# Optimization experiments

Hardware: AMD Instinct MI355X
Metric: run time of the kernel (lower is better)

Reference implementation:

```python
import jax, jax.numpy as jnp
import numpy as np

NUM_HEADS = 32
HEAD_DIM = 128
HIDDEN = NUM_HEADS * HEAD_DIM  # 4096
PAGE_SIZE = 16
NUM_PHYS_PAGES = 512
CACHE_POS = 4096
BATCH = 32
SEQ = 1


def setup_inputs() -> dict:
    key = jax.random.key(0)
    ks = jax.random.split(key, 6)
    scale = 0.02
    x = jax.random.normal(ks[0], (BATCH, SEQ, HIDDEN), dtype=jnp.float32)
    w_qkv = jax.random.normal(ks[1], (HIDDEN, 3 * HIDDEN), dtype=jnp.float32) * scale
    b_qkv = jnp.zeros((3 * HIDDEN,), dtype=jnp.float32)
    w_proj = jax.random.normal(ks[2], (HIDDEN, HIDDEN), dtype=jnp.float32) * scale
    b_proj = jnp.zeros((HIDDEN,), dtype=jnp.float32)
    k_pages = jax.random.normal(ks[3], (NUM_PHYS_PAGES, PAGE_SIZE, NUM_HEADS, HEAD_DIM), dtype=jnp.float32)
    v_pages = jax.random.normal(ks[4], (NUM_PHYS_PAGES, PAGE_SIZE, NUM_HEADS, HEAD_DIM), dtype=jnp.float32)
    # logical page -> physical page mapping (page table for one request)
    page_table = jax.random.randint(ks[5], (CACHE_POS // PAGE_SIZE,), 0, NUM_PHYS_PAGES, dtype=jnp.int64)
    return {
        "x": x, "w_qkv": w_qkv, "b_qkv": b_qkv, "w_proj": w_proj, "b_proj": b_proj,
        "k_pages": k_pages, "v_pages": v_pages, "page_table": page_table,
        "cache_pos": CACHE_POS,
    }


def reference(x, w_qkv, b_qkv, w_proj, b_proj, k_pages, v_pages, page_table, cache_pos):
    B, S, H = x.shape
    # fused QKV projection
    qkv = x @ w_qkv + b_qkv                      # [B,S,3H]
    q, k, v = jnp.split(qkv, 3, axis=-1)
    q = q.reshape(B, S, NUM_HEADS, HEAD_DIM).transpose(0, 2, 1, 3)  # [B,Hh,S,D]
    k = k.reshape(B, S, NUM_HEADS, HEAD_DIM).transpose(0, 2, 1, 3)
    v = v.reshape(B, S, NUM_HEADS, HEAD_DIM).transpose(0, 2, 1, 3)

    # Paged KV-cache gather: position -> (physical page, local offset)
    pos = jnp.arange(cache_pos)                  # cache_pos is a static Python int
    phys = page_table[pos // PAGE_SIZE]          # [T]
    off = pos % PAGE_SIZE                        # [T]
    cached_k = k_pages[phys, off]                # [T, Hh, D]
    cached_v = v_pages[phys, off]                # [T, Hh, D]
    # [1,Hh,T,D], shared across batch (as in the torch expand)
    cached_k = jnp.transpose(cached_k, (1, 0, 2))[None]
    cached_v = jnp.transpose(cached_v, (1, 0, 2))[None]
    cached_k = jnp.broadcast_to(cached_k, (B,) + cached_k.shape[1:])
    cached_v = jnp.broadcast_to(cached_v, (B,) + cached_v.shape[1:])

    k_full = jnp.concatenate([cached_k, k], axis=2)  # [B,Hh,T+S,D]
    v_full = jnp.concatenate([cached_v, v], axis=2)

    scores = jnp.einsum('bhsd,bhtd->bhst', q, k_full) / (HEAD_DIM ** 0.5)
    attn = jax.nn.softmax(scores, axis=-1)
    out = jnp.einsum('bhst,bhtd->bhsd', attn, v_full)  # [B,Hh,S,D]
    out = out.transpose(0, 2, 1, 3).reshape(B, S, H)
    return out @ w_proj + b_proj
```

## Files before the change

### kernel.cpp

```cpp
#include <hip/hip_runtime.h>

typedef __attribute__((ext_vector_type(4))) float f32x4;
typedef __attribute__((ext_vector_type(8))) short short8;
typedef unsigned short u16;
typedef unsigned int u32;

#define HEADS 32
#define D 128
#define TCACHE 4096
#define HID 4096
#define QKVN 12288
#define TSPLIT 32
#define KPS (TCACHE / TSPLIT)
#define QKV_KSPLIT 4
#define PROJ_KSPLIT 8
#define SCALE 0.08838834764831845f
#define ARENA_W 10880

static __device__ __forceinline__ float bf2f(u16 u) {
  u32 v = ((u32)u) << 16;
  return __builtin_bit_cast(float, v);
}
static __device__ __forceinline__ u16 f2bf(float f) {
  u32 u = __builtin_bit_cast(u32, f);
  u += 0x7FFFu + ((u >> 16) & 1u);
  return (u16)(u >> 16);
}

template <bool BF>
static __device__ __forceinline__ short8 load8(const void* p, long idx) {
  if constexpr (BF) {
    return *(const short8*)((const u16*)p + idx);
  } else {
    const float* f = (const float*)p + idx;
    f32x4 a = *(const f32x4*)f;
    f32x4 b = *(const f32x4*)(f + 4);
    short8 r;
    r[0] = (short)f2bf(a[0]); r[1] = (short)f2bf(a[1]);
    r[2] = (short)f2bf(a[2]); r[3] = (short)f2bf(a[3]);
    r[4] = (short)f2bf(b[0]); r[5] = (short)f2bf(b[1]);
    r[6] = (short)f2bf(b[2]); r[7] = (short)f2bf(b[3]);
    return r;
  }
}
template <bool BF>
static __device__ __forceinline__ short ld1(const void* p, long idx) {
  if constexpr (BF) return (short)((const u16*)p)[idx];
  else return (short)f2bf(((const float*)p)[idx]);
}

__global__ void prep(const u32* __restrict__ x, const u32* __restrict__ raw,
                     int* __restrict__ flag, int* __restrict__ ptn) {
  if (blockIdx.x == 0) {
    __shared__ int cnt;
    if (threadIdx.x == 0) cnt = 0;
    __syncthreads();
    u32 v = x[threadIdx.x * 256];
    u32 e = (v >> 7) & 0xFF;
    if (e >= 110 && e <= 140) atomicAdd(&cnt, 1);
    __syncthreads();
    if (threadIdx.x == 0) *flag = (cnt >= 192) ? 1 : 0;
  } else {
    __shared__ int is64;
    if (threadIdx.x == 0) is64 = 1;
    __syncthreads();
    if (threadIdx.x < 128) {
      u32 odd = raw[2 * threadIdx.x + 1];
      if (odd != 0) atomicAnd(&is64, 0);
    }
    __syncthreads();
    if (is64) ptn[threadIdx.x] = (int)raw[2 * threadIdx.x];
    else ptn[threadIdx.x] = (int)raw[threadIdx.x];
  }
}

template <bool ABF, bool BBF>
static __device__ __forceinline__ void gemm_body(const void* __restrict__ A,
                                                 const void* __restrict__ B,
                                                 float* __restrict__ C, int K, int N) {
  int wave = threadIdx.x >> 6, lane = threadIdx.x & 63;
  int l16 = lane & 15, lg = lane >> 4;
  int n0 = blockIdx.x * 64 + wave * 16;
  int kper = K / gridDim.y;
  int k0 = blockIdx.y * kper;
  f32x4 acc0 = {0.f, 0.f, 0.f, 0.f}, acc1 = {0.f, 0.f, 0.f, 0.f};
  long arow0 = (long)l16 * K, arow1 = (long)(l16 + 16) * K;
#pragma unroll 4
  for (int kk = k0; kk < k0 + kper; kk += 32) {
    long kbase = kk + lg * 8;
    short8 a0 = load8<ABF>(A, arow0 + kbase);
    short8 a1 = load8<ABF>(A, arow1 + kbase);
    short8 bfr;
#pragma unroll
    for (int i = 0; i < 8; i++) bfr[i] = ld1<BBF>(B, (kbase + i) * (long)N + n0 + l16);
    acc0 = __builtin_amdgcn_mfma_f32_16x16x32_bf16(a0, bfr, acc0, 0, 0, 0);
    acc1 = __builtin_amdgcn_mfma_f32_16x16x32_bf16(a1, bfr, acc1, 0, 0, 0);
  }
  float* Co = C + (long)blockIdx.y * 32 * N;
#pragma unroll
  for (int i = 0; i < 4; i++) {
    int b = lg * 4 + i;
    Co[(long)b * N + n0 + l16] = acc0[i];
    Co[(long)(b + 16) * N + n0 + l16] = acc1[i];
  }
}

#define GPITCH 36
static __device__ __forceinline__ void gemm32_body(const float* __restrict__ A,
                                                   const float* __restrict__ B,
                                                   float* __restrict__ C, int K, int N,
                                                   u16* __restrict__ BtL,
                                                   u16* __restrict__ AtL) {
  int t = threadIdx.x;
  int wave = t >> 6, lane = t & 63, l16 = lane & 15, lg = lane >> 4;
  int kper = K / gridDim.y;
  int k0 = blockIdx.y * kper;
  int steps = kper >> 5;
  long n0 = (long)blockIdx.x * 64;
  int bk = (t >> 4) * 2;
  int bc = (t & 15) * 4;
  int am = t >> 3;
  int ak = (t & 7) * 4;
  f32x4 acc0 = {0.f, 0.f, 0.f, 0.f}, acc1 = {0.f, 0.f, 0.f, 0.f};
  f32x4 rb0, rb1, ra;

  auto LOADG = [&](int kk) {
    const float* Bp = B + (long)(k0 + kk + bk) * N + n0 + bc;
    rb0 = *(const f32x4*)Bp;
    rb1 = *(const f32x4*)(Bp + N);
    ra = *(const f32x4*)(A + (long)am * K + k0 + kk + ak);
  };
  auto STORE = [&](int buf) {
    u16* Bt = BtL + buf * (64 * GPITCH);
#pragma unroll
    for (int c = 0; c < 4; c++) {
      u32 w = (u32)f2bf(rb0[c]) | ((u32)f2bf(rb1[c]) << 16);
      *(u32*)(Bt + (bc + c) * GPITCH + bk) = w;
    }
    u16* At = AtL + buf * (32 * GPITCH);
    *(u32*)(At + am * GPITCH + ak) = (u32)f2bf(ra[0]) | ((u32)f2bf(ra[1]) << 16);
    *(u32*)(At + am * GPITCH + ak + 2) = (u32)f2bf(ra[2]) | ((u32)f2bf(ra[3]) << 16);
  };
  auto FRAGMFMA = [&](int buf) {
    union { short8 s8; u32 w[4]; } bf, af0, af1;
    const u32* bp = (const u32*)(BtL + buf * (64 * GPITCH) + ((wave * 16 + l16) * GPITCH + lg * 8));
    bf.w[0] = bp[0]; bf.w[1] = bp[1]; bf.w[2] = bp[2]; bf.w[3] = bp[3];
    const u32* a0p = (const u32*)(AtL + buf * (32 * GPITCH) + (l16 * GPITCH + lg * 8));
    af0.w[0] = a0p[0]; af0.w[1] = a0p[1]; af0.w[2] = a0p[2]; af0.w[3] = a0p[3];
    const u32* a1p = (const u32*)(AtL + buf * (32 * GPITCH) + ((l16 + 16) * GPITCH + lg * 8));
    af1.w[0] = a1p[0]; af1.w[1] = a1p[1]; af1.w[2] = a1p[2]; af1.w[3] = a1p[3];
    acc0 = __builtin_amdgcn_mfma_f32_16x16x32_bf16(af0.s8, bf.s8, acc0, 0, 0, 0);
    acc1 = __builtin_amdgcn_mfma_f32_16x16x32_bf16(af1.s8, bf.s8, acc1, 0, 0, 0);
  };

  LOADG(0);
  STORE(0);
  __syncthreads();
  for (int s = 0; s < steps; s++) {
    int cur = s & 1;
    bool more = (s + 1 < steps);
    if (more) LOADG((s + 1) * 32);
    FRAGMFMA(cur);
    if (more) STORE(cur ^ 1);
    __syncthreads();
  }
  float* Co = C + (long)blockIdx.y * 32 * N;
  long cw = n0 + wave * 16 + l16;
#pragma unroll
  for (int i = 0; i < 4; i++) {
    int b = lg * 4 + i;
    Co[(long)b * N + cw] = acc0[i];
    Co[(long)(b + 16) * N + cw] = acc1[i];
  }
}

__global__ __launch_bounds__(256) void qkv_gemm(const void* A, const void* B, float* C,
                                                const int* flag) {
  __shared__ u16 BtL[2 * 64 * GPITCH];
  __shared__ u16 AtL[2 * 32 * GPITCH];
  if (*flag) gemm_body<true, true>(A, B, C, HID, QKVN);
  else gemm32_body((const float*)A, (const float*)B, C, HID, QKVN, BtL, AtL);
}
__global__ __launch_bounds__(256) void proj_gemm(const void* Abf, const void* Af32,
                                                 const void* B, float* C, const int* flag) {
  __shared__ u16 BtL[2 * 64 * GPITCH];
  __shared__ u16 AtL[2 * 32 * GPITCH];
  if (*flag) gemm_body<true, true>(Abf, B, C, HID, HID);
  else gemm32_body((const float*)Af32, (const float*)B, C, HID, HID, BtL, AtL);
}

__global__ void qkv_fin(const float* __restrict__ C, const void* __restrict__ bias,
                        u16* __restrict__ out, const int* __restrict__ flag) {
  int idx = blockIdx.x * 256 + threadIdx.x;
  if (idx >= 32 * QKVN) return;
  int n = idx % QKVN;
  float s = 0.f;
#pragma unroll
  for (int sp = 0; sp < QKV_KSPLIT; sp++) s += C[(long)sp * 32 * QKVN + idx];
  float bv;
  if (*flag) bv = bf2f(((const u16*)bias)[n]);
  else bv = ((const float*)bias)[n];
  out[idx] = f2bf(s + bv);
}

__global__ void proj_fin(const float* __restrict__ C, const void* __restrict__ bias,
                         void* __restrict__ out, const int* __restrict__ flag) {
  int idx = blockIdx.x * 256 + threadIdx.x;
  if (idx >= 32 * HID) return;
  int n = idx % HID;
  float s = 0.f;
#pragma unroll
  for (int sp = 0; sp < PROJ_KSPLIT; sp++) s += C[(long)sp * 32 * HID + idx];
  if (*flag) {
    s += bf2f(((const u16*)bias)[n]);
    ((u16*)out)[idx] = f2bf(s);
  } else {
    s += ((const float*)bias)[n];
    ((float*)out)[idx] = s;
  }
}

template <bool BF>
static __device__ __forceinline__ void attn_body(const u16* __restrict__ qkv,
                                                 const void* __restrict__ kp,
                                                 const void* __restrict__ vp,
                                                 const int* __restrict__ pt,
                                                 float* __restrict__ Op,
                                                 float* __restrict__ mp,
                                                 float* __restrict__ lp,
                                                 char* __restrict__ arena,
                                                 float (*mL)[32], float (*lL)[32]) {
  int split = blockIdx.x, h = blockIdx.y;
  int wave = threadIdx.x >> 6, lane = threadIdx.x & 63;
  int l16 = lane & 15, lg = lane >> 4;
  u16* VLw = (u16*)(arena + wave * ARENA_W);
  u16* pldsw = (u16*)(arena + wave * ARENA_W + 8320);

  short8 qf[2][4];
#pragma unroll
  for (int mt = 0; mt < 2; mt++)
#pragma unroll
    for (int ks = 0; ks < 4; ks++)
      qf[mt][ks] = *(const short8*)(qkv + (long)(l16 + 16 * mt) * QKVN + h * D + ks * 32 + lg * 8);

  f32x4 acc[2][8];
#pragma unroll
  for (int mt = 0; mt < 2; mt++)
#pragma unroll
    for (int nt = 0; nt < 8; nt++) acc[mt][nt] = f32x4{0.f, 0.f, 0.f, 0.f};
  float mrun[2][4], lrun[2][4];

  int tbase = split * KPS + wave * 32;
  int tb16 = tbase >> 4;
  int pg0 = pt[tb16], pg1 = pt[tb16 + 1];

#pragma unroll
  for (int p = 0; p < 2; p++) {
    int kc = (lane >> 2) + p * 16;
    int dq = (lane & 3) * 32;
    int pg = (kc & 16) ? pg1 : pg0;
    long vr = ((long)(pg * 16 + (kc & 15)) * HEADS + h) * D;
    u32 w[16];
    if constexpr (BF) {
      const u32* src = (const u32*)vp + ((vr + dq) >> 1);
#pragma unroll
      for (int j = 0; j < 16; j++) w[j] = src[j];
    } else {
      const float* src = (const float*)vp + vr + dq;
#pragma unroll
      for (int j = 0; j < 8; j++) {
        f32x4 tv = *(const f32x4*)(src + j * 4);
        w[2 * j] = (u32)f2bf(tv[0]) | ((u32)f2bf(tv[1]) << 16);
        w[2 * j + 1] = (u32)f2bf(tv[2]) | ((u32)f2bf(tv[3]) << 16);
      }
    }
    u32* dst = (u32*)(VLw + kc * 130 + dq);
#pragma unroll
    for (int j = 0; j < 16; j++) dst[j] = w[j];
  }

  f32x4 sacc[2][2];
#pragma unroll
  for (int kt = 0; kt < 2; kt++)
#pragma unroll
    for (int mt = 0; mt < 2; mt++) sacc[kt][mt] = f32x4{0.f, 0.f, 0.f, 0.f};
#pragma unroll
  for (int kt = 0; kt < 2; kt++) {
    long krow = ((long)((kt ? pg1 : pg0) * 16 + l16) * HEADS + h) * D;
#pragma unroll
    for (int ks = 0; ks < 4; ks++) {
      short8 kf = load8<BF>(kp, krow + ks * 32 + lg * 8);
      sacc[kt][0] = __builtin_amdgcn_mfma_f32_16x16x32_bf16(qf[0][ks], kf, sacc[kt][0], 0, 0, 0);
      sacc[kt][1] = __builtin_amdgcn_mfma_f32_16x16x32_bf16(qf[1][ks], kf, sacc[kt][1], 0, 0, 0);
    }
  }

  float p[2][2][4];
#pragma unroll
  for (int mt = 0; mt < 2; mt++) {
#pragma unroll
    for (int i = 0; i < 4; i++) {
      float s0 = sacc[0][mt][i] * SCALE, s1 = sacc[1][mt][i] * SCALE;
      float mx = fmaxf(s0, s1);
      mx = fmaxf(mx, __shfl_xor(mx, 1));
      mx = fmaxf(mx, __shfl_xor(mx, 2));
      mx = fmaxf(mx, __shfl_xor(mx, 4));
      mx = fmaxf(mx, __shfl_xor(mx, 8));
      float p0 = __expf(s0 - mx), p1 = __expf(s1 - mx);
      float ps = p0 + p1;
      ps += __shfl_xor(ps, 1);
      ps += __shfl_xor(ps, 2);
      ps += __shfl_xor(ps, 4);
      ps += __shfl_xor(ps, 8);
      mrun[mt][i] = mx;
      lrun[mt][i] = ps;
      p[0][mt][i] = p0;
      p[1][mt][i] = p1;
    }
  }

#pragma unroll
  for (int kt = 0; kt < 2; kt++)
#pragma unroll
    for (int mt = 0; mt < 2; mt++)
#pragma unroll
      for (int i = 0; i < 4; i++)
        pldsw[(lg * 4 + i + 16 * mt) * 40 + kt * 16 + l16] = f2bf(p[kt][mt][i]);

  __syncthreads();

  short8 pf0 = *(const short8*)&pldsw[l16 * 40 + lg * 8];
  short8 pf1 = *(const short8*)&pldsw[(l16 + 16) * 40 + lg * 8];

#pragma unroll
  for (int nt = 0; nt < 8; nt++) {
    short8 vf;
#pragma unroll
    for (int i = 0; i < 8; i++) vf[i] = (short)VLw[(lg * 8 + i) * 130 + nt * 16 + l16];
    acc[0][nt] = __builtin_amdgcn_mfma_f32_16x16x32_bf16(pf0, vf, acc[0][nt], 0, 0, 0);
    acc[1][nt] = __builtin_amdgcn_mfma_f32_16x16x32_bf16(pf1, vf, acc[1][nt], 0, 0, 0);
  }

  __syncthreads();

  u16* accw = (u16*)(arena + wave * ARENA_W);
#pragma unroll
  for (int mt = 0; mt < 2; mt++)
#pragma unroll
    for (int i = 0; i < 4; i++) {
      int b = lg * 4 + i + 16 * mt;
#pragma unroll
      for (int nt = 0; nt < 8; nt++) accw[b * D + nt * 16 + l16] = f2bf(acc[mt][nt][i]);
      if (l16 == 0) {
        mL[wave][b] = mrun[mt][i];
        lL[wave][b] = lrun[mt][i];
      }
    }
  __syncthreads();

  long sb = ((long)h * TSPLIT + split) * 32;
  {
    int t = threadIdx.x;
    int b = t >> 3, sub = t & 7;
    float m0 = mL[0][b], m1 = mL[1][b], m2 = mL[2][b], m3 = mL[3][b];
    float ms = fmaxf(fmaxf(m0, m1), fmaxf(m2, m3));
    float w0 = __expf(m0 - ms), w1 = __expf(m1 - ms);
    float w2 = __expf(m2 - ms), w3 = __expf(m3 - ms);
    float ls = lL[0][b] * w0 + lL[1][b] * w1 + lL[2][b] * w2 + lL[3][b] * w3;
    const u16* a0 = (const u16*)(arena);
    const u16* a1 = (const u16*)(arena + ARENA_W);
    const u16* a2 = (const u16*)(arena + 2 * ARENA_W);
    const u16* a3 = (const u16*)(arena + 3 * ARENA_W);
    long ob = (sb + b) * (long)D;
#pragma unroll
    for (int j = 0; j < 16; j++) {
      int d = sub + 8 * j;
      int idx = b * D + d;
      float o = bf2f(a0[idx]) * w0 + bf2f(a1[idx]) * w1 + bf2f(a2[idx]) * w2 + bf2f(a3[idx]) * w3;
      Op[ob + d] = o;
    }
    if (sub == 0) {
      mp[sb + b] = ms;
      lp[sb + b] = ls;
    }
  }
}

__global__ __launch_bounds__(256) void attn_partial(const u16* qkv, const void* kp,
                                                    const void* vp, const int* pt,
                                                    const int* flag, float* Op, float* mp,
                                                    float* lp) {
  __shared__ __align__(16) char arena[4 * ARENA_W];
  __shared__ float mL[4][32], lL[4][32];
  if (*flag) attn_body<true>(qkv, kp, vp, pt, Op, mp, lp, arena, mL, lL);
  else attn_body<false>(qkv, kp, vp, pt, Op, mp, lp, arena, mL, lL);
}

__global__ __launch_bounds__(64) void attn_combine(const u16* __restrict__ qkv,
                                                   const float* __restrict__ Op,
                                                   const float* __restrict__ mp,
                                                   const float* __restrict__ lp,
                                                   u16* __restrict__ aout,
                                                   float* __restrict__ aoutf) {
  int bh = blockIdx.x;
  int b = bh >> 5, h = bh & 31;
  int lane = threadIdx.x;
  long qb = (long)b * QKVN + h * D + 2 * lane;
  float q0 = bf2f(qkv[qb]), q1 = bf2f(qkv[qb + 1]);
  float k0 = bf2f(qkv[qb + HID]), k1 = bf2f(qkv[qb + HID + 1]);
  float v0 = bf2f(qkv[qb + 2 * HID]), v1 = bf2f(qkv[qb + 2 * HID + 1]);
  float dot = q0 * k0 + q1 * k1;
#pragma unroll
  for (int m = 1; m < 64; m <<= 1) dot += __shfl_xor(dot, m);
  float scur = dot * SCALE;
  long base = (long)h * TSPLIT * 32 + b;
  float M = scur;
#pragma unroll
  for (int s = 0; s < TSPLIT; s++) M = fmaxf(M, mp[base + s * 32]);
  float w = __expf(scur - M), L = w, o0 = w * v0, o1 = w * v1;
#pragma unroll
  for (int s = 0; s < TSPLIT; s++) {
    float wsx = __expf(mp[base + s * 32] - M);
    L += lp[base + s * 32] * wsx;
    const float* o = Op + (base + s * 32) * D + 2 * lane;
    o0 += wsx * o[0];
    o1 += wsx * o[1];
  }
  float inv = 1.0f / L;
  o0 *= inv;
  o1 *= inv;
  long oi = (long)b * HID + h * D + 2 * lane;
  u32 pk = (u32)f2bf(o0) | ((u32)f2bf(o1) << 16);
  *(u32*)(aout + oi) = pk;
  aoutf[oi] = o0;
  aoutf[oi + 1] = o1;
}

extern "C" void kernel_launch(void* const* d_in, const int* in_sizes, int n_in, void* d_out,
                              int out_size, void* d_ws, size_t ws_size, hipStream_t stream) {
  const void* x = d_in[0];
  const void* wqkv = d_in[1];
  const void* bqkv = d_in[2];
  const void* wproj = d_in[3];
  const void* bproj = d_in[4];
  const void* kp = d_in[5];
  const void* vp = d_in[6];
  const u32* ptraw = (const u32*)d_in[7];

  char* wsb = (char*)d_ws;
  int* flag = (int*)(wsb + 0);
  int* ptn = (int*)(wsb + 16);
  float* qkv_part = (float*)(wsb + 2048);
  float* proj_part = qkv_part;
  float* attn_f32 = (float*)(wsb + 2048 + 4194304);
  u16* qkv_bf = (u16*)(wsb + 6293504);
  float* Opart = (float*)(wsb + 7079936);
  float* mpart = (float*)(wsb + 23857152);
  float* lpart = (float*)(wsb + 23988224);
  u16* attn_bf = (u16*)(wsb + 24119296);

  prep<<<2, 256, 0, stream>>>((const u32*)x, ptraw, flag, ptn);
  qkv_gemm<<<dim3(QKVN / 64, QKV_KSPLIT), 256, 0, stream>>>(x, wqkv, qkv_part, flag);
  qkv_fin<<<(32 * QKVN) / 256, 256, 0, stream>>>(qkv_part, bqkv, qkv_bf, flag);
  attn_partial<<<dim3(TSPLIT, HEADS), 256, 0, stream>>>(qkv_bf, kp, vp, ptn, flag, Opart,
                                                        mpart, lpart);
  attn_combine<<<32 * 32, 64, 0, stream>>>(qkv_bf, Opart, mpart, lpart, attn_bf, attn_f32);
  proj_gemm<<<dim3(HID / 64, PROJ_KSPLIT), 256, 0, stream>>>(attn_bf, attn_f32, wproj,
                                                             proj_part, flag);
  proj_fin<<<(32 * HID) / 256, 256, 0, stream>>>(proj_part, bproj, d_out, flag);
}
```

Before: 118.0 us.

## Fold prep into QKV GEMM and store attention partials as bf16

The separate prep kernel goes away. Every QKV GEMM block now recomputes the input-dtype flag itself with wave ballots, and block (0,0) also writes the normalized page table and the flag for later kernels. The attention partial outputs are packed as bf16 pairs instead of fp32, which halves partial-output write and combine read traffic. In exchange, the partial outputs lose precision, and every GEMM block does a small extra strided read of the input.

```diff
diff --git a/kernel.cpp b/kernel.cpp
--- a/kernel.cpp
+++ b/kernel.cpp
@@ -47,31 +47,6 @@
 static __device__ __forceinline__ short ld1(const void* p, long idx) {
   if constexpr (BF) return (short)((const u16*)p)[idx];
   else return (short)f2bf(((const float*)p)[idx]);
-}
-
-__global__ void prep(const u32* __restrict__ x, const u32* __restrict__ raw,
-                     int* __restrict__ flag, int* __restrict__ ptn) {
-  if (blockIdx.x == 0) {
-    __shared__ int cnt;
-    if (threadIdx.x == 0) cnt = 0;
-    __syncthreads();
-    u32 v = x[threadIdx.x * 256];
-    u32 e = (v >> 7) & 0xFF;
-    if (e >= 110 && e <= 140) atomicAdd(&cnt, 1);
-    __syncthreads();
-    if (threadIdx.x == 0) *flag = (cnt >= 192) ? 1 : 0;
-  } else {
-    __shared__ int is64;
-    if (threadIdx.x == 0) is64 = 1;
-    __syncthreads();
-    if (threadIdx.x < 128) {
-      u32 odd = raw[2 * threadIdx.x + 1];
-      if (odd != 0) atomicAnd(&is64, 0);
-    }
-    __syncthreads();
-    if (is64) ptn[threadIdx.x] = (int)raw[2 * threadIdx.x];
-    else ptn[threadIdx.x] = (int)raw[threadIdx.x];
-  }
 }
 
 template <bool ABF, bool BBF>
@@ -175,12 +150,34 @@
 }
 
 __global__ __launch_bounds__(256) void qkv_gemm(const void* A, const void* B, float* C,
-                                                const int* flag) {
+                                                const u32* ptraw, int* flag, int* ptn) {
+  __shared__ int wcnt[4];
+  __shared__ int w64[4];
   __shared__ u16 BtL[2 * 64 * GPITCH];
   __shared__ u16 AtL[2 * 32 * GPITCH];
-  if (*flag) gemm_body<true, true>(A, B, C, HID, QKVN);
+  {
+    u32 v = ((const u32*)A)[threadIdx.x * 256];
+    u32 e = (v >> 7) & 0xFF;
+    unsigned long long b = __ballot(e >= 110 && e <= 140);
+    if ((threadIdx.x & 63) == 0) wcnt[threadIdx.x >> 6] = __popcll(b);
+  }
+  bool prep_block = (blockIdx.x == 0) && (blockIdx.y == 0);
+  if (prep_block) {
+    u32 ov = (threadIdx.x < 128) ? ptraw[2 * threadIdx.x + 1] : 0u;
+    unsigned long long b2 = __ballot(ov != 0u);
+    if ((threadIdx.x & 63) == 0) w64[threadIdx.x >> 6] = (b2 != 0ull) ? 1 : 0;
+  }
+  __syncthreads();
+  int f = (wcnt[0] + wcnt[1] + wcnt[2] + wcnt[3]) >= 192;
+  if (prep_block) {
+    int is64 = !(w64[0] | w64[1] | w64[2] | w64[3]);
+    ptn[threadIdx.x] = is64 ? (int)ptraw[2 * threadIdx.x] : (int)ptraw[threadIdx.x];
+    if (threadIdx.x == 0) *flag = f;
+  }
+  if (f) gemm_body<true, true>(A, B, C, HID, QKVN);
   else gemm32_body((const float*)A, (const float*)B, C, HID, QKVN, BtL, AtL);
 }
+
 __global__ __launch_bounds__(256) void proj_gemm(const void* Abf, const void* Af32,
                                                  const void* B, float* C, const int* flag) {
   __shared__ u16 BtL[2 * 64 * GPITCH];
@@ -225,7 +222,7 @@
                                                  const void* __restrict__ kp,
                                                  const void* __restrict__ vp,
                                                  const int* __restrict__ pt,
-                                                 float* __restrict__ Op,
+                                                 u32* __restrict__ Op16,
                                                  float* __restrict__ mp,
                                                  float* __restrict__ lp,
                                                  char* __restrict__ arena,
@@ -367,17 +364,21 @@
     float w0 = __expf(m0 - ms), w1 = __expf(m1 - ms);
     float w2 = __expf(m2 - ms), w3 = __expf(m3 - ms);
     float ls = lL[0][b] * w0 + lL[1][b] * w1 + lL[2][b] * w2 + lL[3][b] * w3;
-    const u16* a0 = (const u16*)(arena);
-    const u16* a1 = (const u16*)(arena + ARENA_W);
-    const u16* a2 = (const u16*)(arena + 2 * ARENA_W);
-    const u16* a3 = (const u16*)(arena + 3 * ARENA_W);
-    long ob = (sb + b) * (long)D;
-#pragma unroll
-    for (int j = 0; j < 16; j++) {
-      int d = sub + 8 * j;
-      int idx = b * D + d;
-      float o = bf2f(a0[idx]) * w0 + bf2f(a1[idx]) * w1 + bf2f(a2[idx]) * w2 + bf2f(a3[idx]) * w3;
-      Op[ob + d] = o;
+    const u32* a0 = (const u32*)(arena);
+    const u32* a1 = (const u32*)(arena + ARENA_W);
+    const u32* a2 = (const u32*)(arena + 2 * ARENA_W);
+    const u32* a3 = (const u32*)(arena + 3 * ARENA_W);
+    u32* Oprow = Op16 + (sb + b) * 64;
+#pragma unroll
+    for (int j = 0; j < 8; j++) {
+      int w = sub + 8 * j;
+      int idx = b * 64 + w;
+      u32 x0 = a0[idx], x1 = a1[idx], x2 = a2[idx], x3 = a3[idx];
+      float lo = bf2f((u16)(x0 & 0xFFFF)) * w0 + bf2f((u16)(x1 & 0xFFFF)) * w1 +
+                 bf2f((u16)(x2 & 0xFFFF)) * w2 + bf2f((u16)(x3 & 0xFFFF)) * w3;
+      float hi = bf2f((u16)(x0 >> 16)) * w0 + bf2f((u16)(x1 >> 16)) * w1 +
+                 bf2f((u16)(x2 >> 16)) * w2 + bf2f((u16)(x3 >> 16)) * w3;
+      Oprow[w] = (u32)f2bf(lo) | ((u32)f2bf(hi) << 16);
     }
     if (sub == 0) {
       mp[sb + b] = ms;
@@ -388,16 +389,16 @@
 
 __global__ __launch_bounds__(256) void attn_partial(const u16* qkv, const void* kp,
                                                     const void* vp, const int* pt,
-                                                    const int* flag, float* Op, float* mp,
+                                                    const int* flag, u32* Op16, float* mp,
                                                     float* lp) {
   __shared__ __align__(16) char arena[4 * ARENA_W];
   __shared__ float mL[4][32], lL[4][32];
-  if (*flag) attn_body<true>(qkv, kp, vp, pt, Op, mp, lp, arena, mL, lL);
-  else attn_body<false>(qkv, kp, vp, pt, Op, mp, lp, arena, mL, lL);
+  if (*flag) attn_body<true>(qkv, kp, vp, pt, Op16, mp, lp, arena, mL, lL);
+  else attn_body<false>(qkv, kp, vp, pt, Op16, mp, lp, arena, mL, lL);
 }
 
 __global__ __launch_bounds__(64) void attn_combine(const u16* __restrict__ qkv,
-                                                   const float* __restrict__ Op,
+                                                   const u32* __restrict__ Op16,
                                                    const float* __restrict__ mp,
                                                    const float* __restrict__ lp,
                                                    u16* __restrict__ aout,
@@ -422,9 +423,9 @@
   for (int s = 0; s < TSPLIT; s++) {
     float wsx = __expf(mp[base + s * 32] - M);
     L += lp[base + s * 32] * wsx;
-    const float* o = Op + (base + s * 32) * D + 2 * lane;
-    o0 += wsx * o[0];
-    o1 += wsx * o[1];
+    u32 x = Op16[(base + s * 32) * 64 + lane];
+    o0 += wsx * bf2f((u16)(x & 0xFFFF));
+    o1 += wsx * bf2f((u16)(x >> 16));
   }
   float inv = 1.0f / L;
   o0 *= inv;
@@ -454,17 +455,17 @@
   float* proj_part = qkv_part;
   float* attn_f32 = (float*)(wsb + 2048 + 4194304);
   u16* qkv_bf = (u16*)(wsb + 6293504);
-  float* Opart = (float*)(wsb + 7079936);
-  float* mpart = (float*)(wsb + 23857152);
-  float* lpart = (float*)(wsb + 23988224);
-  u16* attn_bf = (u16*)(wsb + 24119296);
-
-  prep<<<2, 256, 0, stream>>>((const u32*)x, ptraw, flag, ptn);
-  qkv_gemm<<<dim3(QKVN / 64, QKV_KSPLIT), 256, 0, stream>>>(x, wqkv, qkv_part, flag);
+  u32* Opart16 = (u32*)(wsb + 7079936);
+  float* mpart = (float*)(wsb + 15468544);
+  float* lpart = (float*)(wsb + 15599616);
+  u16* attn_bf = (u16*)(wsb + 15730688);
+
+  qkv_gemm<<<dim3(QKVN / 64, QKV_KSPLIT), 256, 0, stream>>>(x, wqkv, qkv_part, ptraw, flag,
+                                                            ptn);
   qkv_fin<<<(32 * QKVN) / 256, 256, 0, stream>>>(qkv_part, bqkv, qkv_bf, flag);
-  attn_partial<<<dim3(TSPLIT, HEADS), 256, 0, stream>>>(qkv_bf, kp, vp, ptn, flag, Opart,
+  attn_partial<<<dim3(TSPLIT, HEADS), 256, 0, stream>>>(qkv_bf, kp, vp, ptn, flag, Opart16,
                                                         mpart, lpart);
-  attn_combine<<<32 * 32, 64, 0, stream>>>(qkv_bf, Opart, mpart, lpart, attn_bf, attn_f32);
+  attn_combine<<<32 * 32, 64, 0, stream>>>(qkv_bf, Opart16, mpart, lpart, attn_bf, attn_f32);
   proj_gemm<<<dim3(HID / 64, PROJ_KSPLIT), 256, 0, stream>>>(attn_bf, attn_f32, wproj,
                                                              proj_part, flag);
   proj_fin<<<(32 * HID) / 256, 256, 0, stream>>>(proj_part, bproj, d_out, flag);
```

Result: faster. 111.6 us (-5.4%).
